# Kernel tuning notes

Hardware: AMD Instinct MI355X
Metric: run time of the kernel (lower is better)

Reference implementation:

```python
import jax, jax.numpy as jnp
import numpy as np
from jax import lax

B, S, E, H, V, C = 256, 128, 512, 1024, 128, 18


def setup_inputs() -> dict:
    key = jax.random.key(0)
    ks = jax.random.split(key, 12)
    x_in = jax.random.randint(ks[0], (B, S), 0, V, dtype=jnp.int64)
    x_lengths = jax.random.randint(ks[1], (B,), 1, S + 1, dtype=jnp.int64)
    emb = jax.random.normal(ks[2], (V, E), dtype=jnp.float32) * 0.05
    emb = emb.at[0].set(0.0)  # padding_idx=0
    W_ih = jax.random.normal(ks[3], (H, E), dtype=jnp.float32) * (1.0 / np.sqrt(H))
    b_ih = jax.random.normal(ks[4], (H,), dtype=jnp.float32) * 0.01
    W_hh = jax.random.normal(ks[5], (H, H), dtype=jnp.float32) * (1.0 / np.sqrt(H))
    b_hh = jax.random.normal(ks[6], (H,), dtype=jnp.float32) * 0.01
    W1 = jax.random.normal(ks[7], (H, H), dtype=jnp.float32) * (1.0 / np.sqrt(H))
    b1 = jax.random.normal(ks[8], (H,), dtype=jnp.float32) * 0.01
    W2 = jax.random.normal(ks[9], (C, H), dtype=jnp.float32) * (1.0 / np.sqrt(H))
    b2 = jax.random.normal(ks[10], (C,), dtype=jnp.float32) * 0.01
    return {"x_in": x_in, "x_lengths": x_lengths, "emb": emb,
            "W_ih": W_ih, "b_ih": b_ih, "W_hh": W_hh, "b_hh": b_hh,
            "W1": W1, "b1": b1, "W2": W2, "b2": b2}


def reference(x_in, x_lengths, emb, W_ih, b_ih, W_hh, b_hh, W1, b1, W2, b2):
    # Embedding lookup: [B, S, E]
    x = emb[x_in]
    # Precompute the input-to-hidden projection for all timesteps: [S, B, H]
    pre = jnp.einsum('bse,he->sbh', x, W_ih) + b_ih

    def step(h, p_t):
        h_new = jnp.tanh(p_t + h @ W_hh.T + b_hh)
        return h_new, h_new

    h0 = jnp.zeros((x.shape[0], W_hh.shape[0]), dtype=x.dtype)
    _, hiddens = lax.scan(step, h0, pre)          # [S, B, H]
    hiddens = jnp.transpose(hiddens, (1, 0, 2))   # [B, S, H]

    # column_gather: final hidden state per sequence length
    idx = (x_lengths - 1).astype(jnp.int32)
    last = hiddens[jnp.arange(hiddens.shape[0]), idx]  # [B, H]

    # MLP head (dropout treated as identity / eval mode)
    y = jax.nn.relu(last @ W1.T + b1)
    return y @ W2.T + b2
```

## Files before the change

kernel.cpp:

```cpp
#include <hip/hip_runtime.h>
#include <hip/hip_bf16.h>

#define BB 256
#define SS 128
#define EE 512
#define HH 1024
#define VV 128
#define CC 18

typedef _Float16 f16x8 __attribute__((ext_vector_type(8)));
typedef _Float16 f16x4 __attribute__((ext_vector_type(4)));
typedef float    f32x4 __attribute__((ext_vector_type(4)));

#define HBUF_OFF  0x000000
#define FLAGS_OFF 0x200000
#define EP_OFF    0x210000
#define LAST_OFF  0x290000
#define Z_OFF     0x390000

__device__ inline f16x8 cvt8(f32x4 a, f32x4 b) {
  f16x8 r;
  r[0] = (_Float16)a.x; r[1] = (_Float16)a.y; r[2] = (_Float16)a.z; r[3] = (_Float16)a.w;
  r[4] = (_Float16)b.x; r[5] = (_Float16)b.y; r[6] = (_Float16)b.z; r[7] = (_Float16)b.w;
  return r;
}

__device__ inline f16x8 ld_cp16(const _Float16* p) {
  const unsigned long long* q = (const unsigned long long*)p;
  union { unsigned long long u[2]; f16x8 v; } r;
  r.u[0] = __hip_atomic_load(q + 0, __ATOMIC_RELAXED, __HIP_MEMORY_SCOPE_AGENT);
  r.u[1] = __hip_atomic_load(q + 1, __ATOMIC_RELAXED, __HIP_MEMORY_SCOPE_AGENT);
  return r.v;
}
__device__ inline void st_cp8(_Float16* p, f16x4 v) {
  union { f16x4 v; unsigned long long u; } c; c.v = v;
  __hip_atomic_store((unsigned long long*)p, c.u, __ATOMIC_RELAXED,
                     __HIP_MEMORY_SCOPE_AGENT);
}

__global__ __launch_bounds__(256) void k_embproj(const float* __restrict__ emb,
                                                 const float* __restrict__ W_ih,
                                                 const float* __restrict__ b_ih,
                                                 const float* __restrict__ b_hh,
                                                 float* __restrict__ ep) {
  __shared__ float red[4][16][66];
  const int bid = blockIdx.x;
  const int v0 = (bid & 7) * 16;
  const int h0 = (bid >> 3) * 64;
  const int tid = threadIdx.x;
  const int w = tid >> 6, lane = tid & 63, lr = lane & 15, lk = lane >> 4;

  f32x4 acc[4] = {};
  const int vrow = v0 + lr;
#pragma unroll
  for (int ki = 0; ki < 4; ++ki) {
    const int k = w * 128 + ki * 32 + lk * 8;
    const f32x4* pa = (const f32x4*)(emb + vrow * EE + k);
    f16x8 af = cvt8(pa[0], pa[1]);
#pragma unroll
    for (int nt = 0; nt < 4; ++nt) {
      const int hcol = h0 + nt * 16 + lr;
      const f32x4* pb = (const f32x4*)(W_ih + hcol * EE + k);
      f16x8 bf = cvt8(pb[0], pb[1]);
      acc[nt] = __builtin_amdgcn_mfma_f32_16x16x32_f16(af, bf, acc[nt], 0, 0, 0);
    }
  }
#pragma unroll
  for (int nt = 0; nt < 4; ++nt)
#pragma unroll
    for (int j = 0; j < 4; ++j)
      red[w][lk * 4 + j][nt * 16 + lr] = acc[nt][j];
  __syncthreads();

  const int r = tid >> 4, cg = tid & 15, cc0 = cg * 4;
  const int vvr = v0 + r;
#pragma unroll
  for (int i = 0; i < 4; ++i) {
    const int hcol = h0 + cc0 + i;
    float s = red[0][r][cc0 + i] + red[1][r][cc0 + i] +
              red[2][r][cc0 + i] + red[3][r][cc0 + i];
    ep[vvr * HH + hcol] = s + b_ih[hcol] + b_hh[hcol];
  }
}

__global__ __launch_bounds__(256) void k_rnn(const float* __restrict__ W_hh,
                                             const int* __restrict__ x_in,
                                             const int* __restrict__ x_len,
                                             const float* __restrict__ ep,
                                             _Float16* __restrict__ hbuf,
                                             int* __restrict__ flags,
                                             float* __restrict__ lastb) {
  __shared__ float red[4][16][66];
  __shared__ int xin[16][128];
  __shared__ int len1[16];

  const int bid = blockIdx.x;
  const int g = bid & 15;
  const int c = bid >> 4;
  const int row0 = g * 16, col0 = c * 64;
  const int tid = threadIdx.x;
  const int w = tid >> 6, lane = tid & 63, lr = lane & 15, lk = lane >> 4;

  for (int i = tid; i < 16 * SS; i += 256) {
    const int r = i >> 7, s = i & 127;
    xin[r][s] = x_in[(row0 + r) * SS + s];
  }
  if (tid < 16) len1[tid] = x_len[row0 + tid] - 1;

  f16x8 wreg[4][8];
#pragma unroll
  for (int nt = 0; nt < 4; ++nt) {
    const int col = col0 + nt * 16 + lr;
#pragma unroll
    for (int ki = 0; ki < 8; ++ki) {
      const int k = w * 256 + ki * 32 + lk * 8;
      const f32x4* pw = (const f32x4*)(W_hh + col * HH + k);
      wreg[nt][ki] = cvt8(pw[0], pw[1]);
    }
  }
  __syncthreads();

  int gmax = 0;
#pragma unroll
  for (int r16 = 0; r16 < 16; ++r16) gmax = max(gmax, len1[r16]);

  const int arow = row0 + lr;
  const int r = tid >> 4, cc0 = (tid & 15) * 4;
  for (int t = 0; t <= gmax; ++t) {
    const int bufR = t & 1;
    const _Float16* hr_hi = hbuf + ((size_t)(bufR * 2 + 0) * BB + arow) * HH;
    const _Float16* hr_lo = hbuf + ((size_t)(bufR * 2 + 1) * BB + arow) * HH;

    f32x4 acch[4] = {};
    f32x4 accl[4] = {};
#pragma unroll
    for (int ki = 0; ki < 8; ++ki) {
      const int k = w * 256 + ki * 32 + lk * 8;
      f16x8 ahi = ld_cp16(hr_hi + k);
      f16x8 alo = ld_cp16(hr_lo + k);
#pragma unroll
      for (int nt = 0; nt < 4; ++nt) {
        acch[nt] = __builtin_amdgcn_mfma_f32_16x16x32_f16(ahi, wreg[nt][ki], acch[nt], 0, 0, 0);
        accl[nt] = __builtin_amdgcn_mfma_f32_16x16x32_f16(alo, wreg[nt][ki], accl[nt], 0, 0, 0);
      }
    }
#pragma unroll
    for (int nt = 0; nt < 4; ++nt)
#pragma unroll
      for (int j = 0; j < 4; ++j)
        red[w][lk * 4 + j][nt * 16 + lr] = acch[nt][j] + accl[nt][j] * (1.0f / 4096.0f);

    const int vv = xin[r][t];
    const f32x4 pre4 = *(const f32x4*)(ep + vv * HH + col0 + cc0);
    __syncthreads();

    float sv[4];
#pragma unroll
    for (int i = 0; i < 4; ++i)
      sv[i] = red[0][r][cc0 + i] + red[1][r][cc0 + i] +
              red[2][r][cc0 + i] + red[3][r][cc0 + i];

    float th[4];
#pragma unroll
    for (int i = 0; i < 4; ++i) {
      const float x = sv[i] + ((i == 0) ? pre4.x : (i == 1) ? pre4.y : (i == 2) ? pre4.z : pre4.w);
      const float e = __expf(-2.0f * fabsf(x));
      th[i] = copysignf((1.0f - e) / (1.0f + e), x);
    }

    const int bufW = bufR ^ 1;
    const int grow = row0 + r;
    f16x4 h4, l4;
#pragma unroll
    for (int i = 0; i < 4; ++i) {
      const _Float16 hh = (_Float16)th[i];
      h4[i] = hh;
      l4[i] = (_Float16)((th[i] - (float)hh) * 4096.0f);
    }

    if (len1[r] == t) {
      f32x4 o; o.x = th[0]; o.y = th[1]; o.z = th[2]; o.w = th[3];
      *(f32x4*)(lastb + (size_t)grow * HH + col0 + cc0) = o;
    }

    if (t < gmax) {
      st_cp8(hbuf + ((size_t)(bufW * 2 + 0) * BB + grow) * HH + col0 + cc0, h4);
      st_cp8(hbuf + ((size_t)(bufW * 2 + 1) * BB + grow) * HH + col0 + cc0, l4);

      __syncthreads();
      if (tid == 0) {
        __hip_atomic_fetch_add(&flags[g * SS + t], 1, __ATOMIC_RELAXED,
                               __HIP_MEMORY_SCOPE_AGENT);
        while (__hip_atomic_load(&flags[g * SS + t], __ATOMIC_RELAXED,
                                 __HIP_MEMORY_SCOPE_AGENT) < 16) {
          __builtin_amdgcn_s_sleep(1);
        }
      }
      __syncthreads();
      asm volatile("" ::: "memory");
    }
  }
}

__global__ __launch_bounds__(256) void k_mlp1(const float* __restrict__ lastb,
                                              const float* __restrict__ W1,
                                              const float* __restrict__ b1,
                                              float* __restrict__ z) {
  __shared__ float red[4][16][66];
  const int bid = blockIdx.x;
  const int row0 = (bid & 15) * 16, col0 = (bid >> 4) * 64;
  const int tid = threadIdx.x;
  const int w = tid >> 6, lane = tid & 63, lr = lane & 15, lk = lane >> 4;
  const int arow = row0 + lr;

  f32x4 acch[4] = {};
  f32x4 accl[4] = {};
#pragma unroll
  for (int ki = 0; ki < 8; ++ki) {
    const int k = w * 256 + ki * 32 + lk * 8;
    const f32x4* pa = (const f32x4*)(lastb + (size_t)arow * HH + k);
    f32x4 a0 = pa[0], a1 = pa[1];
    f16x8 ahi, alo;
#pragma unroll
    for (int i = 0; i < 4; ++i) {
      float v0 = (i == 0) ? a0.x : (i == 1) ? a0.y : (i == 2) ? a0.z : a0.w;
      float v1 = (i == 0) ? a1.x : (i == 1) ? a1.y : (i == 2) ? a1.z : a1.w;
      _Float16 h0 = (_Float16)v0, h1 = (_Float16)v1;
      ahi[i] = h0; ahi[i + 4] = h1;
      alo[i] = (_Float16)((v0 - (float)h0) * 4096.0f);
      alo[i + 4] = (_Float16)((v1 - (float)h1) * 4096.0f);
    }
#pragma unroll
    for (int nt = 0; nt < 4; ++nt) {
      const int colw = col0 + nt * 16 + lr;
      const f32x4* pb = (const f32x4*)(W1 + (size_t)colw * HH + k);
      f16x8 bf = cvt8(pb[0], pb[1]);
      acch[nt] = __builtin_amdgcn_mfma_f32_16x16x32_f16(ahi, bf, acch[nt], 0, 0, 0);
      accl[nt] = __builtin_amdgcn_mfma_f32_16x16x32_f16(alo, bf, accl[nt], 0, 0, 0);
    }
  }
#pragma unroll
  for (int nt = 0; nt < 4; ++nt)
#pragma unroll
    for (int j = 0; j < 4; ++j)
      red[w][lk * 4 + j][nt * 16 + lr] = acch[nt][j] + accl[nt][j] * (1.0f / 4096.0f);
  __syncthreads();

  const int r = tid >> 4, cc0 = (tid & 15) * 4;
  const int grow = row0 + r;
#pragma unroll
  for (int i = 0; i < 4; ++i) {
    const int col = col0 + cc0 + i;
    float s = red[0][r][cc0 + i] + red[1][r][cc0 + i] +
              red[2][r][cc0 + i] + red[3][r][cc0 + i] + b1[col];
    z[(size_t)grow * HH + col] = fmaxf(s, 0.0f);
  }
}

__global__ __launch_bounds__(256) void k_mlp2(const float* __restrict__ z,
                                              const float* __restrict__ W2,
                                              const float* __restrict__ b2,
                                              float* __restrict__ out) {
  __shared__ float redy[4][CC];
  const int b = blockIdx.x;
  const int tid = threadIdx.x;
  const int w = tid >> 6, lane = tid & 63;
  const int k = w * 256 + lane * 4;

  const f32x4 z4 = *(const f32x4*)(z + (size_t)b * HH + k);
  float part[CC];
#pragma unroll
  for (int c = 0; c < CC; ++c) {
    const f32x4 w4 = *(const f32x4*)(W2 + (size_t)c * HH + k);
    part[c] = z4.x * w4.x + z4.y * w4.y + z4.z * w4.z + z4.w * w4.w;
  }
#pragma unroll
  for (int c = 0; c < CC; ++c) {
    float v = part[c];
    for (int off = 32; off; off >>= 1) v += __shfl_down(v, off, 64);
    if (lane == 0) redy[w][c] = v;
  }
  __syncthreads();
  if (tid < CC)
    out[b * CC + tid] = redy[0][tid] + redy[1][tid] + redy[2][tid] + redy[3][tid] + b2[tid];
}

extern "C" void kernel_launch(void* const* d_in, const int* in_sizes, int n_in,
                              void* d_out, int out_size, void* d_ws, size_t ws_size,
                              hipStream_t stream) {
  const int*   x_in  = (const int*)d_in[0];
  const int*   x_len = (const int*)d_in[1];
  const float* emb   = (const float*)d_in[2];
  const float* W_ih  = (const float*)d_in[3];
  const float* b_ih  = (const float*)d_in[4];
  const float* W_hh  = (const float*)d_in[5];
  const float* b_hh  = (const float*)d_in[6];
  const float* W1    = (const float*)d_in[7];
  const float* b1    = (const float*)d_in[8];
  const float* W2    = (const float*)d_in[9];
  const float* b2    = (const float*)d_in[10];

  char* ws = (char*)d_ws;
  _Float16* hbuf = (_Float16*)(ws + HBUF_OFF);
  int* flags     = (int*)(ws + FLAGS_OFF);
  float* ep      = (float*)(ws + EP_OFF);
  float* lastb   = (float*)(ws + LAST_OFF);
  float* z       = (float*)(ws + Z_OFF);

  (void)hipMemsetAsync(hbuf, 0, 0x100000, stream);
  (void)hipMemsetAsync(flags, 0, 16 * SS * 4, stream);

  hipLaunchKernelGGL(k_embproj, dim3(128), dim3(256), 0, stream, emb, W_ih, b_ih, b_hh, ep);
  hipLaunchKernelGGL(k_rnn,    dim3(256), dim3(256), 0, stream, W_hh, x_in, x_len, ep, hbuf, flags, lastb);
  hipLaunchKernelGGL(k_mlp1,   dim3(256), dim3(256), 0, stream, lastb, W1, b1, z);
  hipLaunchKernelGGL(k_mlp2,   dim3(256), dim3(256), 0, stream, z, W2, b2, (float*)d_out);
}
```

Before: 768.1 us.

## Replace atomic-counter grid barrier with per-block step flags and peeled first step

Result: slower. 803.4 us (+4.6%).

```diff
diff --git a/kernel.cpp b/kernel.cpp
--- a/kernel.cpp
+++ b/kernel.cpp
@@ -36,6 +36,21 @@
   union { f16x4 v; unsigned long long u; } c; c.v = v;
   __hip_atomic_store((unsigned long long*)p, c.u, __ATOMIC_RELAXED,
                      __HIP_MEMORY_SCOPE_AGENT);
+}
+
+__device__ inline void group_wait(const int* gflags, int lane, int target) {
+  while (true) {
+    int f = __hip_atomic_load(&gflags[lane & 15], __ATOMIC_RELAXED,
+                              __HIP_MEMORY_SCOPE_AGENT);
+    if (__all(f >= target)) break;
+    __builtin_amdgcn_s_sleep(1);
+  }
+  asm volatile("" ::: "memory");
+}
+
+__device__ inline float tanh_fast(float x) {
+  const float e = __expf(-2.0f * fabsf(x));
+  return copysignf((1.0f - e) / (1.0f + e), x);
 }
 
 __global__ __launch_bounds__(256) void k_embproj(const float* __restrict__ emb,
@@ -83,14 +98,14 @@
   }
 }
 
-__global__ __launch_bounds__(256) void k_rnn(const float* __restrict__ W_hh,
-                                             const int* __restrict__ x_in,
-                                             const int* __restrict__ x_len,
-                                             const float* __restrict__ ep,
-                                             _Float16* __restrict__ hbuf,
-                                             int* __restrict__ flags,
-                                             float* __restrict__ lastb) {
-  __shared__ float red[4][16][66];
+__global__ __launch_bounds__(256, 1) void k_rnn(const float* __restrict__ W_hh,
+                                                const int* __restrict__ x_in,
+                                                const int* __restrict__ x_len,
+                                                const float* __restrict__ ep,
+                                                _Float16* __restrict__ hbuf,
+                                                int* __restrict__ flags,
+                                                float* __restrict__ lastb) {
+  __shared__ float red[4][16][68];
   __shared__ int xin[16][128];
   __shared__ int len1[16];
 
@@ -100,10 +115,11 @@
   const int row0 = g * 16, col0 = c * 64;
   const int tid = threadIdx.x;
   const int w = tid >> 6, lane = tid & 63, lr = lane & 15, lk = lane >> 4;
+  int* gflags = flags + g * 16;
 
   for (int i = tid; i < 16 * SS; i += 256) {
-    const int r = i >> 7, s = i & 127;
-    xin[r][s] = x_in[(row0 + r) * SS + s];
+    const int r_ = i >> 7, s_ = i & 127;
+    xin[r_][s_] = x_in[(row0 + r_) * SS + s_];
   }
   if (tid < 16) len1[tid] = x_len[row0 + tid] - 1;
 
@@ -126,22 +142,60 @@
 
   const int arow = row0 + lr;
   const int r = tid >> 4, cc0 = (tid & 15) * 4;
-  for (int t = 0; t <= gmax; ++t) {
+  const int grow = row0 + r;
+
+  {
+    const int vv = xin[r][0];
+    const f32x4 pre4 = *(const f32x4*)(ep + vv * HH + col0 + cc0);
+    float th[4];
+    th[0] = tanh_fast(pre4.x); th[1] = tanh_fast(pre4.y);
+    th[2] = tanh_fast(pre4.z); th[3] = tanh_fast(pre4.w);
+
+    if (len1[r] == 0) {
+      f32x4 o; o.x = th[0]; o.y = th[1]; o.z = th[2]; o.w = th[3];
+      *(f32x4*)(lastb + (size_t)grow * HH + col0 + cc0) = o;
+    }
+    if (gmax >= 1) {
+      f16x4 h4, l4;
+#pragma unroll
+      for (int i = 0; i < 4; ++i) {
+        const _Float16 hh = (_Float16)th[i];
+        h4[i] = hh;
+        l4[i] = (_Float16)((th[i] - (float)hh) * 4096.0f);
+      }
+      st_cp8(hbuf + ((size_t)(1 * 2 + 0) * BB + grow) * HH + col0 + cc0, h4);
+      st_cp8(hbuf + ((size_t)(1 * 2 + 1) * BB + grow) * HH + col0 + cc0, l4);
+      __syncthreads();
+      if (tid == 0)
+        __hip_atomic_store(&gflags[c], 1, __ATOMIC_RELAXED, __HIP_MEMORY_SCOPE_AGENT);
+      group_wait(gflags, lane, 1);
+    }
+  }
+
+  for (int t = 1; t <= gmax; ++t) {
     const int bufR = t & 1;
     const _Float16* hr_hi = hbuf + ((size_t)(bufR * 2 + 0) * BB + arow) * HH;
     const _Float16* hr_lo = hbuf + ((size_t)(bufR * 2 + 1) * BB + arow) * HH;
 
+    const int vv = xin[r][t];
+    const f32x4 pre4 = *(const f32x4*)(ep + vv * HH + col0 + cc0);
+
+    f16x8 ahi[8], alo[8];
+#pragma unroll
+    for (int ki = 0; ki < 8; ++ki) {
+      const int k = w * 256 + ki * 32 + lk * 8;
+      ahi[ki] = ld_cp16(hr_hi + k);
+      alo[ki] = ld_cp16(hr_lo + k);
+    }
+
     f32x4 acch[4] = {};
     f32x4 accl[4] = {};
 #pragma unroll
     for (int ki = 0; ki < 8; ++ki) {
-      const int k = w * 256 + ki * 32 + lk * 8;
-      f16x8 ahi = ld_cp16(hr_hi + k);
-      f16x8 alo = ld_cp16(hr_lo + k);
 #pragma unroll
       for (int nt = 0; nt < 4; ++nt) {
-        acch[nt] = __builtin_amdgcn_mfma_f32_16x16x32_f16(ahi, wreg[nt][ki], acch[nt], 0, 0, 0);
-        accl[nt] = __builtin_amdgcn_mfma_f32_16x16x32_f16(alo, wreg[nt][ki], accl[nt], 0, 0, 0);
+        acch[nt] = __builtin_amdgcn_mfma_f32_16x16x32_f16(ahi[ki], wreg[nt][ki], acch[nt], 0, 0, 0);
+        accl[nt] = __builtin_amdgcn_mfma_f32_16x16x32_f16(alo[ki], wreg[nt][ki], accl[nt], 0, 0, 0);
       }
     }
 #pragma unroll
@@ -149,34 +203,19 @@
 #pragma unroll
       for (int j = 0; j < 4; ++j)
         red[w][lk * 4 + j][nt * 16 + lr] = acch[nt][j] + accl[nt][j] * (1.0f / 4096.0f);
-
-    const int vv = xin[r][t];
-    const f32x4 pre4 = *(const f32x4*)(ep + vv * HH + col0 + cc0);
     __syncthreads();
 
-    float sv[4];
-#pragma unroll
-    for (int i = 0; i < 4; ++i)
-      sv[i] = red[0][r][cc0 + i] + red[1][r][cc0 + i] +
-              red[2][r][cc0 + i] + red[3][r][cc0 + i];
+    const f32x4 s0 = *(const f32x4*)&red[0][r][cc0];
+    const f32x4 s1 = *(const f32x4*)&red[1][r][cc0];
+    const f32x4 s2 = *(const f32x4*)&red[2][r][cc0];
+    const f32x4 s3 = *(const f32x4*)&red[3][r][cc0];
+    const f32x4 sv = (s0 + s1) + (s2 + s3);
 
     float th[4];
-#pragma unroll
-    for (int i = 0; i < 4; ++i) {
-      const float x = sv[i] + ((i == 0) ? pre4.x : (i == 1) ? pre4.y : (i == 2) ? pre4.z : pre4.w);
-      const float e = __expf(-2.0f * fabsf(x));
-      th[i] = copysignf((1.0f - e) / (1.0f + e), x);
-    }
-
-    const int bufW = bufR ^ 1;
-    const int grow = row0 + r;
-    f16x4 h4, l4;
-#pragma unroll
-    for (int i = 0; i < 4; ++i) {
-      const _Float16 hh = (_Float16)th[i];
-      h4[i] = hh;
-      l4[i] = (_Float16)((th[i] - (float)hh) * 4096.0f);
-    }
+    th[0] = tanh_fast(sv.x + pre4.x);
+    th[1] = tanh_fast(sv.y + pre4.y);
+    th[2] = tanh_fast(sv.z + pre4.z);
+    th[3] = tanh_fast(sv.w + pre4.w);
 
     if (len1[r] == t) {
       f32x4 o; o.x = th[0]; o.y = th[1]; o.z = th[2]; o.w = th[3];
@@ -184,20 +223,21 @@
     }
 
     if (t < gmax) {
+      const int bufW = bufR ^ 1;
+      f16x4 h4, l4;
+#pragma unroll
+      for (int i = 0; i < 4; ++i) {
+        const _Float16 hh = (_Float16)th[i];
+        h4[i] = hh;
+        l4[i] = (_Float16)((th[i] - (float)hh) * 4096.0f);
+      }
       st_cp8(hbuf + ((size_t)(bufW * 2 + 0) * BB + grow) * HH + col0 + cc0, h4);
       st_cp8(hbuf + ((size_t)(bufW * 2 + 1) * BB + grow) * HH + col0 + cc0, l4);
 
       __syncthreads();
-      if (tid == 0) {
-        __hip_atomic_fetch_add(&flags[g * SS + t], 1, __ATOMIC_RELAXED,
-                               __HIP_MEMORY_SCOPE_AGENT);
-        while (__hip_atomic_load(&flags[g * SS + t], __ATOMIC_RELAXED,
-                                 __HIP_MEMORY_SCOPE_AGENT) < 16) {
-          __builtin_amdgcn_s_sleep(1);
-        }
-      }
-      __syncthreads();
-      asm volatile("" ::: "memory");
+      if (tid == 0)
+        __hip_atomic_store(&gflags[c], t + 1, __ATOMIC_RELAXED, __HIP_MEMORY_SCOPE_AGENT);
+      group_wait(gflags, lane, t + 1);
     }
   }
 }
@@ -307,8 +347,7 @@
   float* lastb   = (float*)(ws + LAST_OFF);
   float* z       = (float*)(ws + Z_OFF);
 
-  (void)hipMemsetAsync(hbuf, 0, 0x100000, stream);
-  (void)hipMemsetAsync(flags, 0, 16 * SS * 4, stream);
+  (void)hipMemsetAsync(flags, 0, 16 * 16 * 4, stream);
 
   hipLaunchKernelGGL(k_embproj, dim3(128), dim3(256), 0, stream, emb, W_ih, b_ih, b_hh, ep);
   hipLaunchKernelGGL(k_rnn,    dim3(256), dim3(256), 0, stream, W_hh, x_in, x_len, ep, hbuf, flags, lastb);
```
